# Performance work log

Measured on AMD Instinct MI355X. Metric: run time of the kernel, lower is better.

## Reference

```python
import jax, jax.numpy as jnp
import numpy as np

DIM = 64
HEADS = 4
WIN = 4


def setup_inputs() -> dict:
    key = jax.random.key(0)
    ks = jax.random.split(key, 9)
    B, C, D, H, W = 2, DIM, 64, 64, 64
    x = jax.random.normal(ks[0], (B, C, D, H, W), dtype=jnp.float32)
    # 1x1x1 Conv3d == pointwise linear: weight [C_out, C_in], bias [C_out]
    def mk(kw, kb):
        return (jax.random.normal(kw, (C, C), dtype=jnp.float32) * 0.05,
                jax.random.normal(kb, (C,), dtype=jnp.float32) * 0.05)
    Wq, bq = mk(ks[1], ks[2])
    Wk, bk = mk(ks[3], ks[4])
    Wv, bv = mk(ks[5], ks[6])
    Wp, bp = mk(ks[7], ks[8])
    return {"x": x, "Wq": Wq, "bq": bq, "Wk": Wk, "bk": bk,
            "Wv": Wv, "bv": bv, "Wp": Wp, "bp": bp}


def reference(x, Wq, bq, Wk, bk, Wv, bv, Wp, bp):
    B, C, D, H, W = x.shape
    w = WIN
    heads = HEADS
    hd = C // heads
    L = w * w * w  # tokens per window (64)
    nd, nh, nw = D // w, H // w, W // w  # spatial dims are multiples of w -> no padding branch
    scale = hd ** -0.5

    # window partition: [B,C,D,H,W] -> [B*nd*nh*nw, C, L]
    xw = (x.reshape(B, C, nd, w, nh, w, nw, w)
            .transpose(0, 2, 4, 6, 1, 3, 5, 7)
            .reshape(B * nd * nh * nw, C, L))

    def pointwise(t, Wm, bm):  # 1x1x1 conv on flattened windows
        return jnp.einsum('ncl,oc->nol', t, Wm) + bm[None, :, None]

    q = pointwise(xw, Wq, bq).reshape(-1, heads, hd, L)
    k = pointwise(xw, Wk, bk).reshape(-1, heads, hd, L)
    v = pointwise(xw, Wv, bv).reshape(-1, heads, hd, L)

    # attn[n,h,i,j] = <q[:, :, :, i], k[:, :, :, j]> * scale ; softmax over j
    attn = jax.nn.softmax(jnp.einsum('nhdi,nhdj->nhij', q, k) * scale, axis=-1)
    # out = v @ attn^T  (dropout is identity in eval)
    out = jnp.einsum('nhdj,nhij->nhdi', v, attn)

    out = out.reshape(-1, C, L)
    out = pointwise(out, Wp, bp)

    # reverse window partition: [B*nd*nh*nw, C, L] -> [B,C,D,H,W]
    out = (out.reshape(B, nd, nh, nw, C, w, w, w)
              .transpose(0, 4, 1, 5, 2, 6, 3, 7)
              .reshape(B, C, D, H, W))
    return out
```

## Files before the change

### kernel.cpp

```cpp
#include <hip/hip_runtime.h>

typedef _Float16 f16;
typedef __attribute__((ext_vector_type(4))) _Float16 f16x4;
typedef __attribute__((ext_vector_type(8))) _Float16 f16x8;
typedef __attribute__((ext_vector_type(4))) float f32x4;

#define MFMA32(a,b,c) __builtin_amdgcn_mfma_f32_16x16x32_f16((a),(b),(c),0,0,0)
#define MFMA16(a,b,c) __builtin_amdgcn_mfma_f32_16x16x16f16((a),(b),(c),0,0,0)

__global__ __launch_bounds__(256, 2)
void wsa3d(const float* __restrict__ x,
           const float* __restrict__ Wq, const float* __restrict__ bq,
           const float* __restrict__ Wk, const float* __restrict__ bk,
           const float* __restrict__ Wv, const float* __restrict__ bv,
           const float* __restrict__ Wp, const float* __restrict__ bp,
           float* __restrict__ out)
{
    __shared__ __align__(16) f16 lds[32768];
    f16* const XW = lds;
    f16* const PT = lds + 16384;

    const int tid  = threadIdx.x;
    const int lane = tid & 63;
    const int w    = tid >> 6;
    const int g    = lane >> 4;
    const int ln16 = lane & 15;
    const int key  = ln16 & 7;

    const int bid = blockIdx.x;
    const int Q   = ((bid & 7) << 8) | (bid >> 3);
    const int qx = Q & 3, ih = (Q >> 2) & 15, idz = (Q >> 6) & 15, b = Q >> 10;

    const float c_sc = 0.25f * 1.44269504088896340736f;
    const f32x4 z4 = {0.f, 0.f, 0.f, 0.f};

    const int gz = (lane >> 4) & 3, gy = (lane >> 2) & 3, gq = lane & 3;

    f32x4 vals[16];
    #pragma unroll
    for (int i = 0; i < 16; ++i) {
        const int c = w * 16 + i;
        vals[i] = *(const f32x4*)(x + ((((b*64 + c)*64 + idz*4 + gz)*64) + ih*4 + gy)*64 + qx*16 + gq*4);
    }

    {
        const float* Wm[3] = {Wq, Wk, Wv};
        #pragma unroll
        for (int j = 0; j < 12; ++j) {
            const int m   = j >> 2;
            const int row = (j & 3) * 16 + (tid >> 4);
            const int c0  = (tid & 15) * 4;
            f32x4 wv = *(const f32x4*)(Wm[m] + row * 64 + c0);
            f16x4 h4;
            #pragma unroll
            for (int r = 0; r < 4; ++r) h4[r] = (f16)wv[r];
            *(f16x4*)(PT + m*4096 + row*64 + (((c0 >> 3) ^ (row & 7)) << 3) + (c0 & 7)) = h4;
        }
    }

    #pragma unroll
    for (int lx = 0; lx < 4; ++lx) {
        const int t = gz * 16 + gy * 4 + lx;
        #pragma unroll
        for (int h2 = 0; h2 < 2; ++h2) {
            f16x8 pk;
            #pragma unroll
            for (int ii = 0; ii < 8; ++ii) pk[ii] = (f16)vals[h2 * 8 + ii][lx];
            *(f16x8*)(XW + gq*4096 + t*64 + (((w*2 + h2) ^ (t & 7) ^ gq) << 3)) = pk;
        }
    }
    __syncthreads();

    f32x4 bqv[4], bkv[4];
    float bvs[4];
    #pragma unroll
    for (int ob = 0; ob < 4; ++ob) {
        bqv[ob] = *(const f32x4*)(bq + ob * 16 + g * 4);
        bkv[ob] = *(const f32x4*)(bk + ob * 16 + g * 4);
        bvs[ob] = bv[ob * 16 + ln16];
    }

    f16x8 xf[4][2];
    #pragma unroll
    for (int lb = 0; lb < 4; ++lb)
        #pragma unroll
        for (int s = 0; s < 2; ++s)
            xf[lb][s] = *(const f16x8*)(XW + w*4096 + (lb*16 + ln16)*64 + (((g + 4*s) ^ key ^ w) << 3));

    f16x4 qf[4][4], kf[4][4];
    #pragma unroll
    for (int mi = 0; mi < 2; ++mi) {
        #pragma unroll
        for (int ob = 0; ob < 4; ++ob) {
            f16x8 AF[2];
            #pragma unroll
            for (int s = 0; s < 2; ++s)
                AF[s] = *(const f16x8*)(PT + mi*4096 + (ob*16 + ln16)*64 + (((g + 4*s) ^ key) << 3));
            #pragma unroll
            for (int lb = 0; lb < 4; ++lb) {
                f32x4 a = z4;
                #pragma unroll
                for (int s = 0; s < 2; ++s) a = MFMA32(AF[s], xf[lb][s], a);
                f16x4 dst;
                if (mi == 0) {
                    #pragma unroll
                    for (int r = 0; r < 4; ++r) dst[r] = (f16)((a[r] + bqv[ob][r]) * c_sc);
                    qf[ob][lb] = dst;
                } else {
                    #pragma unroll
                    for (int r = 0; r < 4; ++r) dst[r] = (f16)(a[r] + bkv[ob][r]);
                    kf[ob][lb] = dst;
                }
            }
        }
    }

    #pragma unroll
    for (int ob = 0; ob < 4; ++ob) {
        f16x8 VF[2];
        #pragma unroll
        for (int s = 0; s < 2; ++s)
            VF[s] = *(const f16x8*)(PT + 2*4096 + (ob*16 + ln16)*64 + (((g + 4*s) ^ key) << 3));
        #pragma unroll
        for (int tb = 0; tb < 4; ++tb) {
            f32x4 a = z4;
            #pragma unroll
            for (int s = 0; s < 2; ++s) a = MFMA32(xf[tb][s], VF[s], a);
            f16x4 h4;
            #pragma unroll
            for (int r = 0; r < 4; ++r) h4[r] = (f16)(a[r] + bvs[ob]);
            *(f16x4*)(XW + w*4096 + (ob*16 + ln16)*64 + (((2*tb + (g >> 1)) ^ key ^ w) << 3) + 4*(g & 1)) = h4;
        }
    }
    __syncthreads();

    f16x4 ot[4][4];
    #pragma unroll
    for (int h = 0; h < 4; ++h) {
        float invv[4];
        #pragma unroll
        for (int ib = 0; ib < 4; ++ib) {
            f32x4 e[4];
            #pragma unroll
            for (int jb = 0; jb < 4; ++jb) {
                f32x4 S = MFMA16(kf[h][jb], qf[h][ib], z4);
                #pragma unroll
                for (int r = 0; r < 4; ++r) e[jb][r] = __builtin_amdgcn_exp2f(S[r]);
            }
            f32x4 s4 = e[0] + e[1] + e[2] + e[3];
            float hh = (s4[0] + s4[1]) + (s4[2] + s4[3]);
            hh += __shfl_xor(hh, 16);
            hh += __shfl_xor(hh, 32);
            invv[ib] = __builtin_amdgcn_rcpf(hh);
            f16* dst = PT + w*4096 + (ib*16 + ln16)*64;
            #pragma unroll
            for (int jb = 0; jb < 4; ++jb) {
                f16x4 pv;
                #pragma unroll
                for (int r = 0; r < 4; ++r) pv[r] = (f16)e[jb][r];
                *(f16x4*)(dst + (((2*jb + (g >> 1)) ^ key ^ w) << 3) + 4*(g & 1)) = pv;
            }
        }
        f16x8 va[2];
        #pragma unroll
        for (int s = 0; s < 2; ++s)
            va[s] = *(const f16x8*)(XW + w*4096 + (h*16 + ln16)*64 + (((g + 4*s) ^ key ^ w) << 3));
        f32x4 O[4] = {z4, z4, z4, z4};
        #pragma unroll
        for (int s = 0; s < 2; ++s)
            #pragma unroll
            for (int nb = 0; nb < 4; ++nb) {
                f16x8 pb = *(const f16x8*)(PT + w*4096 + (nb*16 + ln16)*64 + (((g + 4*s) ^ key ^ w) << 3));
                O[nb] = MFMA32(va[s], pb, O[nb]);
            }
        #pragma unroll
        for (int nb = 0; nb < 4; ++nb)
            #pragma unroll
            for (int r = 0; r < 4; ++r) ot[h][nb][r] = (f16)(O[nb][r] * invv[nb]);
    }

    #pragma unroll
    for (int h = 0; h < 4; ++h)
        #pragma unroll
        for (int nb = 0; nb < 4; ++nb)
            *(f16x4*)(XW + w*4096 + (nb*16 + ln16)*64 + (((2*h + (g >> 1)) ^ key ^ w) << 3) + 4*(g & 1)) = ot[h][nb];
    __syncthreads();

    #pragma unroll
    for (int j = 0; j < 4; ++j) {
        const int row = j * 16 + (tid >> 4);
        const int c0  = (tid & 15) * 4;
        f32x4 wv = *(const f32x4*)(Wp + row * 64 + c0);
        f16x4 h4;
        #pragma unroll
        for (int r = 0; r < 4; ++r) h4[r] = (f16)wv[r];
        *(f16x4*)(PT + row*64 + (((c0 >> 3) ^ (row & 7)) << 3) + (c0 & 7)) = h4;
    }
    __syncthreads();

    f16x8 wpf[4][2];
    #pragma unroll
    for (int oc = 0; oc < 4; ++oc)
        #pragma unroll
        for (int s = 0; s < 2; ++s)
            wpf[oc][s] = *(const f16x8*)(PT + (oc*16 + ln16)*64 + (((g + 4*s) ^ key) << 3));
    float bps[4];
    #pragma unroll
    for (int oc = 0; oc < 4; ++oc) bps[oc] = bp[oc * 16 + ln16];

    f32x4 res[4][4];
    #pragma unroll
    for (int tb = 0; tb < 4; ++tb) {
        f16x8 af[2];
        #pragma unroll
        for (int s = 0; s < 2; ++s)
            af[s] = *(const f16x8*)(XW + w*4096 + (tb*16 + ln16)*64 + (((g + 4*s) ^ key ^ w) << 3));
        #pragma unroll
        for (int oc = 0; oc < 4; ++oc) {
            f32x4 a = z4;
            #pragma unroll
            for (int s = 0; s < 2; ++s) a = MFMA32(af[s], wpf[oc][s], a);
            #pragma unroll
            for (int r = 0; r < 4; ++r) res[tb][oc][r] = a[r] + bps[oc];
        }
    }

    float* const SG = (float*)(PT + 4096);
    #pragma unroll
    for (int oc = 0; oc < 4; ++oc) {
        #pragma unroll
        for (int tb = 0; tb < 4; ++tb)
            *(f32x4*)(SG + w*1092 + ln16*68 + ((tb*16 + g*4) ^ (w << 2))) = res[tb][oc];
        __syncthreads();
        #pragma unroll
        for (int si = 0; si < 4; ++si) {
            const int o2 = w * 4 + si;
            f32x4 v4 = *(const f32x4*)(SG + gq*1092 + o2*68 + ((gz*16 + gy*4) ^ (gq << 2)));
            *(f32x4*)(out + ((((b*64 + oc*16 + o2)*64 + idz*4 + gz)*64) + ih*4 + gy)*64 + qx*16 + gq*4) = v4;
        }
        if (oc < 3) __syncthreads();
    }
}

extern "C" void kernel_launch(void* const* d_in, const int* in_sizes, int n_in,
                              void* d_out, int out_size, void* d_ws, size_t ws_size,
                              hipStream_t stream) {
    (void)in_sizes; (void)n_in; (void)out_size; (void)d_ws; (void)ws_size;
    const float* x  = (const float*)d_in[0];
    const float* Wq = (const float*)d_in[1];
    const float* bq = (const float*)d_in[2];
    const float* Wk = (const float*)d_in[3];
    const float* bk = (const float*)d_in[4];
    const float* Wv = (const float*)d_in[5];
    const float* bv = (const float*)d_in[6];
    const float* Wp = (const float*)d_in[7];
    const float* bp = (const float*)d_in[8];
    wsa3d<<<2048, 256, 0, stream>>>(x, Wq, bq, Wk, bk, Wv, bv, Wp, bp, (float*)d_out);
}
```

Measured before the change: 74.79 us.

## Pre-convert weights to fp16 fragments and restructure attention to cut LDS and syncs

Adds a tiny prep kernel that converts all four weight matrices to fp16 in MFMA fragment order in workspace, so the main kernel loads fragments straight from global memory instead of staging weights through LDS. Q/K projections are computed per head inside the attention loop, and P·V now uses register-held probabilities with 16x16x16 MFMAs instead of writing P to LDS. LDS use drops and launch bounds rise to 3 blocks per CU, and several barriers are removed. Risks: global fragment loads may be slower than LDS reads, the extra kernel launch adds overhead, and higher occupancy may force register spills.

After: 68.72 us. 1.09x faster.

```diff
diff --git a/kernel.cpp b/kernel.cpp
--- a/kernel.cpp
+++ b/kernel.cpp
@@ -8,17 +8,36 @@
 #define MFMA32(a,b,c) __builtin_amdgcn_mfma_f32_16x16x32_f16((a),(b),(c),0,0,0)
 #define MFMA16(a,b,c) __builtin_amdgcn_mfma_f32_16x16x16f16((a),(b),(c),0,0,0)
 
-__global__ __launch_bounds__(256, 2)
-void wsa3d(const float* __restrict__ x,
-           const float* __restrict__ Wq, const float* __restrict__ bq,
-           const float* __restrict__ Wk, const float* __restrict__ bk,
-           const float* __restrict__ Wv, const float* __restrict__ bv,
-           const float* __restrict__ Wp, const float* __restrict__ bp,
+__global__ void wprep(const float* __restrict__ Wq, const float* __restrict__ Wk,
+                      const float* __restrict__ Wv, const float* __restrict__ Wp,
+                      f16* __restrict__ ws)
+{
+    const int t = threadIdx.x;
+    const int lane = t & 63;
+    const float* Wm[4] = {Wq, Wk, Wv, Wp};
+    #pragma unroll
+    for (int j = 0; j < 8; ++j) {
+        const int c = (t >> 6) * 8 + j;
+        const int m = c >> 3, ob = (c >> 1) & 3, s = c & 1;
+        const float* src = Wm[m] + (ob * 16 + (lane & 15)) * 64 + 8 * (lane >> 4) + 32 * s;
+        f32x4 a4 = *(const f32x4*)src;
+        f32x4 b4 = *(const f32x4*)(src + 4);
+        f16x8 h;
+        #pragma unroll
+        for (int ii = 0; ii < 8; ++ii) h[ii] = (f16)(ii < 4 ? a4[ii] : b4[ii - 4]);
+        *(f16x8*)(ws + c * 512 + lane * 8) = h;
+    }
+}
+
+__global__ __launch_bounds__(256, 3)
+void wsa3d(const float* __restrict__ x, const f16* __restrict__ wsf,
+           const float* __restrict__ bq, const float* __restrict__ bk,
+           const float* __restrict__ bv, const float* __restrict__ bp,
            float* __restrict__ out)
 {
-    __shared__ __align__(16) f16 lds[32768];
-    f16* const XW = lds;
-    f16* const PT = lds + 16384;
+    __shared__ __align__(16) unsigned char smem[50240];
+    f16*   const XW = (f16*)smem;
+    float* const SG = (float*)(smem + 32768);
 
     const int tid  = threadIdx.x;
     const int lane = tid & 63;
@@ -42,22 +61,6 @@
         const int c = w * 16 + i;
         vals[i] = *(const f32x4*)(x + ((((b*64 + c)*64 + idz*4 + gz)*64) + ih*4 + gy)*64 + qx*16 + gq*4);
     }
-
-    {
-        const float* Wm[3] = {Wq, Wk, Wv};
-        #pragma unroll
-        for (int j = 0; j < 12; ++j) {
-            const int m   = j >> 2;
-            const int row = (j & 3) * 16 + (tid >> 4);
-            const int c0  = (tid & 15) * 4;
-            f32x4 wv = *(const f32x4*)(Wm[m] + row * 64 + c0);
-            f16x4 h4;
-            #pragma unroll
-            for (int r = 0; r < 4; ++r) h4[r] = (f16)wv[r];
-            *(f16x4*)(PT + m*4096 + row*64 + (((c0 >> 3) ^ (row & 7)) << 3) + (c0 & 7)) = h4;
-        }
-    }
-
     #pragma unroll
     for (int lx = 0; lx < 4; ++lx) {
         const int t = gz * 16 + gy * 4 + lx;
@@ -71,15 +74,6 @@
     }
     __syncthreads();
 
-    f32x4 bqv[4], bkv[4];
-    float bvs[4];
-    #pragma unroll
-    for (int ob = 0; ob < 4; ++ob) {
-        bqv[ob] = *(const f32x4*)(bq + ob * 16 + g * 4);
-        bkv[ob] = *(const f32x4*)(bk + ob * 16 + g * 4);
-        bvs[ob] = bv[ob * 16 + ln16];
-    }
-
     f16x8 xf[4][2];
     #pragma unroll
     for (int lb = 0; lb < 4; ++lb)
@@ -87,40 +81,12 @@
         for (int s = 0; s < 2; ++s)
             xf[lb][s] = *(const f16x8*)(XW + w*4096 + (lb*16 + ln16)*64 + (((g + 4*s) ^ key ^ w) << 3));
 
-    f16x4 qf[4][4], kf[4][4];
-    #pragma unroll
-    for (int mi = 0; mi < 2; ++mi) {
-        #pragma unroll
-        for (int ob = 0; ob < 4; ++ob) {
-            f16x8 AF[2];
-            #pragma unroll
-            for (int s = 0; s < 2; ++s)
-                AF[s] = *(const f16x8*)(PT + mi*4096 + (ob*16 + ln16)*64 + (((g + 4*s) ^ key) << 3));
-            #pragma unroll
-            for (int lb = 0; lb < 4; ++lb) {
-                f32x4 a = z4;
-                #pragma unroll
-                for (int s = 0; s < 2; ++s) a = MFMA32(AF[s], xf[lb][s], a);
-                f16x4 dst;
-                if (mi == 0) {
-                    #pragma unroll
-                    for (int r = 0; r < 4; ++r) dst[r] = (f16)((a[r] + bqv[ob][r]) * c_sc);
-                    qf[ob][lb] = dst;
-                } else {
-                    #pragma unroll
-                    for (int r = 0; r < 4; ++r) dst[r] = (f16)(a[r] + bkv[ob][r]);
-                    kf[ob][lb] = dst;
-                }
-            }
-        }
-    }
-
     #pragma unroll
     for (int ob = 0; ob < 4; ++ob) {
         f16x8 VF[2];
         #pragma unroll
-        for (int s = 0; s < 2; ++s)
-            VF[s] = *(const f16x8*)(PT + 2*4096 + (ob*16 + ln16)*64 + (((g + 4*s) ^ key) << 3));
+        for (int s = 0; s < 2; ++s) VF[s] = *(const f16x8*)(wsf + (16 + ob*2 + s)*512 + lane*8);
+        const float bvo = bv[ob * 16 + ln16];
         #pragma unroll
         for (int tb = 0; tb < 4; ++tb) {
             f32x4 a = z4;
@@ -128,22 +94,47 @@
             for (int s = 0; s < 2; ++s) a = MFMA32(xf[tb][s], VF[s], a);
             f16x4 h4;
             #pragma unroll
-            for (int r = 0; r < 4; ++r) h4[r] = (f16)(a[r] + bvs[ob]);
+            for (int r = 0; r < 4; ++r) h4[r] = (f16)(a[r] + bvo);
             *(f16x4*)(XW + w*4096 + (ob*16 + ln16)*64 + (((2*tb + (g >> 1)) ^ key ^ w) << 3) + 4*(g & 1)) = h4;
         }
     }
-    __syncthreads();
 
     f16x4 ot[4][4];
     #pragma unroll
     for (int h = 0; h < 4; ++h) {
-        float invv[4];
+        f16x8 QF[2], KF[2];
+        #pragma unroll
+        for (int s = 0; s < 2; ++s) {
+            QF[s] = *(const f16x8*)(wsf + (h*2 + s)*512 + lane*8);
+            KF[s] = *(const f16x8*)(wsf + (8 + h*2 + s)*512 + lane*8);
+        }
+        const f32x4 bqv = *(const f32x4*)(bq + h*16 + g*4);
+        const f32x4 bkv = *(const f32x4*)(bk + h*16 + g*4);
+        f16x4 qf[4], kf[4];
+        #pragma unroll
+        for (int lb = 0; lb < 4; ++lb) {
+            f32x4 aq = z4, ak = z4;
+            #pragma unroll
+            for (int s = 0; s < 2; ++s) {
+                aq = MFMA32(QF[s], xf[lb][s], aq);
+                ak = MFMA32(KF[s], xf[lb][s], ak);
+            }
+            #pragma unroll
+            for (int r = 0; r < 4; ++r) {
+                qf[lb][r] = (f16)((aq[r] + bqv[r]) * c_sc);
+                kf[lb][r] = (f16)(ak[r] + bkv[r]);
+            }
+        }
+        f16x4 va[4];
+        #pragma unroll
+        for (int jb = 0; jb < 4; ++jb)
+            va[jb] = *(const f16x4*)(XW + w*4096 + (16*h + ln16)*64 + (((2*jb + (g >> 1)) ^ key ^ w) << 3) + 4*(g & 1));
         #pragma unroll
         for (int ib = 0; ib < 4; ++ib) {
             f32x4 e[4];
             #pragma unroll
             for (int jb = 0; jb < 4; ++jb) {
-                f32x4 S = MFMA16(kf[h][jb], qf[h][ib], z4);
+                f32x4 S = MFMA16(kf[jb], qf[ib], z4);
                 #pragma unroll
                 for (int r = 0; r < 4; ++r) e[jb][r] = __builtin_amdgcn_exp2f(S[r]);
             }
@@ -151,59 +142,31 @@
             float hh = (s4[0] + s4[1]) + (s4[2] + s4[3]);
             hh += __shfl_xor(hh, 16);
             hh += __shfl_xor(hh, 32);
-            invv[ib] = __builtin_amdgcn_rcpf(hh);
-            f16* dst = PT + w*4096 + (ib*16 + ln16)*64;
+            const float inv = __builtin_amdgcn_rcpf(hh);
+            f32x4 O = z4;
             #pragma unroll
             for (int jb = 0; jb < 4; ++jb) {
-                f16x4 pv;
+                f16x4 pf;
                 #pragma unroll
-                for (int r = 0; r < 4; ++r) pv[r] = (f16)e[jb][r];
-                *(f16x4*)(dst + (((2*jb + (g >> 1)) ^ key ^ w) << 3) + 4*(g & 1)) = pv;
-            }
-        }
-        f16x8 va[2];
-        #pragma unroll
-        for (int s = 0; s < 2; ++s)
-            va[s] = *(const f16x8*)(XW + w*4096 + (h*16 + ln16)*64 + (((g + 4*s) ^ key ^ w) << 3));
-        f32x4 O[4] = {z4, z4, z4, z4};
-        #pragma unroll
-        for (int s = 0; s < 2; ++s)
-            #pragma unroll
-            for (int nb = 0; nb < 4; ++nb) {
-                f16x8 pb = *(const f16x8*)(PT + w*4096 + (nb*16 + ln16)*64 + (((g + 4*s) ^ key ^ w) << 3));
-                O[nb] = MFMA32(va[s], pb, O[nb]);
-            }
-        #pragma unroll
-        for (int nb = 0; nb < 4; ++nb)
-            #pragma unroll
-            for (int r = 0; r < 4; ++r) ot[h][nb][r] = (f16)(O[nb][r] * invv[nb]);
+                for (int r = 0; r < 4; ++r) pf[r] = (f16)e[jb][r];
+                O = MFMA16(va[jb], pf, O);
+            }
+            #pragma unroll
+            for (int r = 0; r < 4; ++r) ot[h][ib][r] = (f16)(O[r] * inv);
+        }
     }
 
     #pragma unroll
     for (int h = 0; h < 4; ++h)
         #pragma unroll
-        for (int nb = 0; nb < 4; ++nb)
-            *(f16x4*)(XW + w*4096 + (nb*16 + ln16)*64 + (((2*h + (g >> 1)) ^ key ^ w) << 3) + 4*(g & 1)) = ot[h][nb];
-    __syncthreads();
-
-    #pragma unroll
-    for (int j = 0; j < 4; ++j) {
-        const int row = j * 16 + (tid >> 4);
-        const int c0  = (tid & 15) * 4;
-        f32x4 wv = *(const f32x4*)(Wp + row * 64 + c0);
-        f16x4 h4;
-        #pragma unroll
-        for (int r = 0; r < 4; ++r) h4[r] = (f16)wv[r];
-        *(f16x4*)(PT + row*64 + (((c0 >> 3) ^ (row & 7)) << 3) + (c0 & 7)) = h4;
-    }
-    __syncthreads();
-
-    f16x8 wpf[4][2];
+        for (int ib = 0; ib < 4; ++ib)
+            *(f16x4*)(XW + w*4096 + (16*ib + ln16)*64 + (((2*h + (g >> 1)) ^ key ^ w) << 3) + 4*(g & 1)) = ot[h][ib];
+
+    f16x8 PF[4][2];
     #pragma unroll
     for (int oc = 0; oc < 4; ++oc)
         #pragma unroll
-        for (int s = 0; s < 2; ++s)
-            wpf[oc][s] = *(const f16x8*)(PT + (oc*16 + ln16)*64 + (((g + 4*s) ^ key) << 3));
+        for (int s = 0; s < 2; ++s) PF[oc][s] = *(const f16x8*)(wsf + (24 + oc*2 + s)*512 + lane*8);
     float bps[4];
     #pragma unroll
     for (int oc = 0; oc < 4; ++oc) bps[oc] = bp[oc * 16 + ln16];
@@ -219,13 +182,12 @@
         for (int oc = 0; oc < 4; ++oc) {
             f32x4 a = z4;
             #pragma unroll
-            for (int s = 0; s < 2; ++s) a = MFMA32(af[s], wpf[oc][s], a);
+            for (int s = 0; s < 2; ++s) a = MFMA32(af[s], PF[oc][s], a);
             #pragma unroll
             for (int r = 0; r < 4; ++r) res[tb][oc][r] = a[r] + bps[oc];
         }
     }
 
-    float* const SG = (float*)(PT + 4096);
     #pragma unroll
     for (int oc = 0; oc < 4; ++oc) {
         #pragma unroll
@@ -245,7 +207,7 @@
 extern "C" void kernel_launch(void* const* d_in, const int* in_sizes, int n_in,
                               void* d_out, int out_size, void* d_ws, size_t ws_size,
                               hipStream_t stream) {
-    (void)in_sizes; (void)n_in; (void)out_size; (void)d_ws; (void)ws_size;
+    (void)in_sizes; (void)n_in; (void)out_size; (void)ws_size;
     const float* x  = (const float*)d_in[0];
     const float* Wq = (const float*)d_in[1];
     const float* bq = (const float*)d_in[2];
@@ -255,5 +217,7 @@
     const float* bv = (const float*)d_in[6];
     const float* Wp = (const float*)d_in[7];
     const float* bp = (const float*)d_in[8];
-    wsa3d<<<2048, 256, 0, stream>>>(x, Wq, bq, Wk, bk, Wv, bv, Wp, bp, (float*)d_out);
+    f16* wsf = (f16*)d_ws;
+    wprep<<<1, 256, 0, stream>>>(Wq, Wk, Wv, Wp, wsf);
+    wsa3d<<<2048, 256, 0, stream>>>(x, wsf, bq, bk, bv, bp, (float*)d_out);
 }
```
